# Optimization experiments

Hardware: AMD Instinct MI355X
Metric: run time of the kernel (lower is better)

## Reference

```python
import jax, jax.numpy as jnp
import numpy as np

N = 4096
D = 1024  # hidden_size == att_size


def setup_inputs() -> dict:
    key = jax.random.key(0)
    ks = jax.random.split(key, 10)
    s = 0.02
    return {
        "q": jax.random.normal(ks[0], (N, D), jnp.float32),
        "k": jax.random.normal(ks[1], (N, D), jnp.float32),
        "v": jax.random.normal(ks[2], (N, D), jnp.float32),
        "bias": jax.random.normal(ks[3], (N, N), jnp.float32) * s,
        "Wq": jax.random.normal(ks[4], (D, D), jnp.float32) * s,
        "bq": jnp.zeros((D,), jnp.float32),
        "Wk": jax.random.normal(ks[5], (D, D), jnp.float32) * s,
        "bk": jnp.zeros((D,), jnp.float32),
        "Wv": jax.random.normal(ks[6], (D, D), jnp.float32) * s,
        "bv": jnp.zeros((D,), jnp.float32),
    }


def reference(q, k, v, bias, Wq, bq, Wk, bk, Wv, bv):
    d = q.shape[-1]
    scale = d ** (-0.5)
    # QKV projections (nn.Linear: x @ W.T + b)
    qp = (q @ Wq.T + bq) * scale          # [N, D]
    kp = k @ Wk.T + bk                    # [N, D]
    vp = v @ Wv.T + bv                    # [N, D]
    # full N x N attention (single head, pseudo-batch of 1 in the original)
    scores = qp @ kp.T                    # [N, N]
    att = jax.nn.softmax(scores, axis=-1) + bias  # POST-softmax bias add
    # dropout is identity in eval mode; original casts weights to fp32 here
    out = att.astype(jnp.float32) @ vp    # [N, D]
    return out
```

## Files before the change

### kernel.cpp

```cpp
#include <hip/hip_runtime.h>
#include <hip/hip_bf16.h>
#include <stdint.h>

typedef unsigned short u16;
using bf16x8 = __attribute__((ext_vector_type(8))) __bf16;
using f32x4  = __attribute__((ext_vector_type(4))) float;

__device__ __forceinline__ u16 f2bf(float f) {
    union { float f; unsigned u; } a; a.f = f;
    unsigned u = a.u;
    u += 0x7fffu + ((u >> 16) & 1u);
    return (u16)(u >> 16);
}
__device__ __forceinline__ float bf2f(unsigned bits_hi16) {
    union { unsigned u; float f; } a; a.u = bits_hi16; return a.f;
}

__device__ __forceinline__ void gload_lds16(const void* g, void* l) {
    __builtin_amdgcn_global_load_lds(
        (const __attribute__((address_space(1))) void*)g,
        (__attribute__((address_space(3))) void*)l, 16, 0, 0);
}

__device__ __forceinline__ void xcd_swz(int nx, int ny, int& x, int& y, int& z) {
    const int flat = (int)blockIdx.x + nx * ((int)blockIdx.y + ny * (int)blockIdx.z);
    const int cpx = (nx * ny * (int)gridDim.z) >> 3;
    const int s = (flat & 7) * cpx + (flat >> 3);
    x = s % nx;
    const int t = s / nx;
    y = t % ny;
    z = t / ny;
}

__device__ __forceinline__ void gemm_core(const u16* __restrict__ A,
                                          const u16* __restrict__ B,
                                          int lda, int ldb, int kLen,
                                          int bm, int bn,
                                          u16* sA, u16* sB,
                                          f32x4 acc[4][4])
{
    const int tid  = threadIdx.x;
    const int lane = tid & 63;
    const int wm   = (tid >> 7) & 1;
    const int wn   = (tid >> 6) & 1;

    const u16* Ag0 = A + (long)(bm * 128 + (tid >> 2)) * lda + (tid & 3) * 8;
    const u16* Ag1 = Ag0 + (long)64 * lda;
    const u16* Bg0 = B + (long)(bn * 128 + (tid >> 2)) * ldb + (tid & 3) * 8;
    const u16* Bg1 = Bg0 + (long)64 * ldb;
    u16* la = sA + tid * 8;
    u16* lb = sB + tid * 8;

    const int rfo = (wm * 64 + (lane & 15)) * 32 + (lane >> 4) * 8;
    const int rfoB = (wn * 64 + (lane & 15)) * 32 + (lane >> 4) * 8;

    for (int k0 = 0; k0 < kLen; k0 += 64) {
        gload_lds16(Ag0 + k0, la);
        gload_lds16(Ag1 + k0, la + 2048);
        gload_lds16(Bg0 + k0, lb);
        gload_lds16(Bg1 + k0, lb + 2048);
        gload_lds16(Ag0 + k0 + 32, la + 4096);
        gload_lds16(Ag1 + k0 + 32, la + 6144);
        gload_lds16(Bg0 + k0 + 32, lb + 4096);
        gload_lds16(Bg1 + k0 + 32, lb + 6144);
        __syncthreads();
#pragma unroll
        for (int h = 0; h < 2; h++) {
            const u16* ra = sA + h * 4096 + rfo;
            const u16* rb = sB + h * 4096 + rfoB;
            bf16x8 af[4], bfr[4];
#pragma unroll
            for (int i = 0; i < 4; i++) af[i]  = *(const bf16x8*)(ra + i * 512);
#pragma unroll
            for (int i = 0; i < 4; i++) bfr[i] = *(const bf16x8*)(rb + i * 512);
#pragma unroll
            for (int mi = 0; mi < 4; mi++)
#pragma unroll
                for (int ni = 0; ni < 4; ni++)
                    acc[mi][ni] = __builtin_amdgcn_mfma_f32_16x16x32_bf16(
                        af[mi], bfr[ni], acc[mi][ni], 0, 0, 0);
        }
        __syncthreads();
    }
}

__global__ __launch_bounds__(256)
void cast6(const float* __restrict__ q, const float* __restrict__ k,
           const float* __restrict__ v, const float* __restrict__ wq,
           const float* __restrict__ wk, const float* __restrict__ wv,
           u16* __restrict__ qb, u16* __restrict__ kb, u16* __restrict__ vb,
           u16* __restrict__ wqb, u16* __restrict__ wkb, u16* __restrict__ wvb,
           int nqkv, int nw)
{
    const int z = blockIdx.y;
    const float* s; u16* d; int n;
    switch (z) {
        case 0:  s = q;  d = qb;  n = nqkv; break;
        case 1:  s = k;  d = kb;  n = nqkv; break;
        case 2:  s = v;  d = vb;  n = nqkv; break;
        case 3:  s = wq; d = wqb; n = nw;   break;
        case 4:  s = wk; d = wkb; n = nw;   break;
        default: s = wv; d = wvb; n = nw;   break;
    }
    long i = ((long)blockIdx.x * 256 + threadIdx.x) * 8;
    if (i >= n) return;
    float4 a = *(const float4*)(s + i);
    float4 b = *(const float4*)(s + i + 4);
    ushort4 o0, o1;
    o0.x = f2bf(a.x); o0.y = f2bf(a.y); o0.z = f2bf(a.z); o0.w = f2bf(a.w);
    o1.x = f2bf(b.x); o1.y = f2bf(b.y); o1.z = f2bf(b.z); o1.w = f2bf(b.w);
    *(ushort4*)(d + i)     = o0;
    *(ushort4*)(d + i + 4) = o1;
}

__global__ __launch_bounds__(256, 2)
void proj_gemm(const u16* __restrict__ qb, const u16* __restrict__ kb,
               const u16* __restrict__ vb, const u16* __restrict__ wqb,
               const u16* __restrict__ wkb, const u16* __restrict__ wvb,
               const float* __restrict__ bq, const float* __restrict__ bk,
               const float* __restrict__ bv,
               u16* __restrict__ qp, u16* __restrict__ kp, u16* __restrict__ vpT)
{
    __shared__ __align__(16) u16 sA[8192];
    __shared__ __align__(16) u16 sB[8192];
    int bx, by, bz;
    xcd_swz(8, 32, bx, by, bz);
    const int z = bz;
    const u16* A = (z == 0) ? qb : (z == 1) ? kb : vb;
    const u16* B = (z == 0) ? wqb : (z == 1) ? wkb : wvb;
    const float* bias = (z == 0) ? bq : (z == 1) ? bk : bv;
    u16* OUT = (z == 0) ? qp : (z == 1) ? kp : vpT;
    const float scale = (z == 0) ? 0.03125f : 1.0f;

    f32x4 acc[4][4] = {};
    gemm_core(A, B, 1024, 1024, 1024, by, bx, sA, sB, acc);

    const int lane = threadIdx.x & 63;
    const int wm   = (threadIdx.x >> 7) & 1;
    const int wn   = (threadIdx.x >> 6) & 1;
    const int m0 = by * 128 + wm * 64 + ((lane >> 4) << 2);
    const int n0 = bx * 128 + wn * 64 + (lane & 15);
#pragma unroll
    for (int mi = 0; mi < 4; mi++)
#pragma unroll
        for (int ni = 0; ni < 4; ni++) {
            const int gm = m0 + mi * 16;
            const int gn = n0 + ni * 16;
            const float bb = bias[gn];
#pragma unroll
            for (int r = 0; r < 4; r++) {
                float val = (acc[mi][ni][r] + bb) * scale;
                if (z < 2) OUT[(long)(gm + r) * 1024 + gn] = f2bf(val);
                else       OUT[(long)gn * 4096 + gm + r]   = f2bf(val);
            }
        }
}

__global__ __launch_bounds__(256, 2)
void vproj_gemm(const u16* __restrict__ wvb, const u16* __restrict__ vb,
                const float* __restrict__ bv, u16* __restrict__ vpT)
{
    __shared__ __align__(16) u16 sA[8192];
    __shared__ __align__(16) u16 sB[8192];
    f32x4 acc[4][4] = {};
    gemm_core(wvb, vb, 1024, 1024, 1024, blockIdx.y, blockIdx.x, sA, sB, acc);

    const int lane = threadIdx.x & 63;
    const int wm   = (threadIdx.x >> 7) & 1;
    const int wn   = (threadIdx.x >> 6) & 1;
    const int m0 = blockIdx.y * 128 + wm * 64 + ((lane >> 4) << 2);
    const int n0 = blockIdx.x * 128 + wn * 64 + (lane & 15);
#pragma unroll
    for (int mi = 0; mi < 4; mi++)
#pragma unroll
        for (int ni = 0; ni < 4; ni++) {
            const int gm = m0 + mi * 16;
            const int gn = n0 + ni * 16;
#pragma unroll
            for (int r = 0; r < 4; r++)
                vpT[(long)(gm + r) * 4096 + gn] = f2bf(acc[mi][ni][r] + bv[gm + r]);
        }
}

__global__ __launch_bounds__(256, 2)
void score_gemm(const u16* __restrict__ qp, const u16* __restrict__ kp,
                u16* __restrict__ S)
{
    __shared__ __align__(16) u16 sA[8192];
    __shared__ __align__(16) u16 sB[8192];
    f32x4 acc[4][4] = {};
    gemm_core(qp, kp, 1024, 1024, 1024, blockIdx.y, blockIdx.x, sA, sB, acc);

    const int lane = threadIdx.x & 63;
    const int wm   = (threadIdx.x >> 7) & 1;
    const int wn   = (threadIdx.x >> 6) & 1;
    const int m0 = blockIdx.y * 128 + wm * 64 + ((lane >> 4) << 2);
    const int n0 = blockIdx.x * 128 + wn * 64 + (lane & 15);
#pragma unroll
    for (int mi = 0; mi < 4; mi++)
#pragma unroll
        for (int ni = 0; ni < 4; ni++) {
            const int gm = m0 + mi * 16;
            const int gn = n0 + ni * 16;
#pragma unroll
            for (int r = 0; r < 4; r++)
                S[(long)(gm + r) * 4096 + gn] = f2bf(acc[mi][ni][r]);
        }
}

__global__ __launch_bounds__(256)
void softmax_bias(const u16* __restrict__ S, const float* __restrict__ bias,
                  u16* __restrict__ att)
{
    const long row = blockIdx.x;
    const int tid = threadIdx.x;
    const u16* srow = S + row * 4096 + tid * 16;

    float v[16];
    {
        uint4 a = *(const uint4*)(srow);
        uint4 b = *(const uint4*)(srow + 8);
        unsigned w[8] = {a.x, a.y, a.z, a.w, b.x, b.y, b.z, b.w};
#pragma unroll
        for (int i = 0; i < 8; i++) {
            v[2 * i]     = bf2f(w[i] << 16);
            v[2 * i + 1] = bf2f(w[i] & 0xffff0000u);
        }
    }
    float mx = v[0];
#pragma unroll
    for (int i = 1; i < 16; i++) mx = fmaxf(mx, v[i]);
#pragma unroll
    for (int o = 32; o >= 1; o >>= 1) mx = fmaxf(mx, __shfl_xor(mx, o, 64));
    __shared__ float red[8];
    if ((tid & 63) == 0) red[tid >> 6] = mx;
    __syncthreads();
    mx = fmaxf(fmaxf(red[0], red[1]), fmaxf(red[2], red[3]));
    float sum = 0.f;
#pragma unroll
    for (int i = 0; i < 16; i++) { v[i] = __expf(v[i] - mx); sum += v[i]; }
#pragma unroll
    for (int o = 32; o >= 1; o >>= 1) sum += __shfl_xor(sum, o, 64);
    if ((tid & 63) == 0) red[4 + (tid >> 6)] = sum;
    __syncthreads();
    const float inv = 1.0f / (red[4] + red[5] + red[6] + red[7]);

    const float4* brow = (const float4*)(bias + row * 4096 + tid * 16);
    unsigned o[8];
#pragma unroll
    for (int i = 0; i < 4; i++) {
        float4 b = brow[i];
        unsigned lo = f2bf(v[4 * i + 0] * inv + b.x);
        unsigned hi = f2bf(v[4 * i + 1] * inv + b.y);
        o[2 * i] = lo | (hi << 16);
        lo = f2bf(v[4 * i + 2] * inv + b.z);
        hi = f2bf(v[4 * i + 3] * inv + b.w);
        o[2 * i + 1] = lo | (hi << 16);
    }
    u16* arow = att + row * 4096 + tid * 16;
    *(uint4*)(arow)     = make_uint4(o[0], o[1], o[2], o[3]);
    *(uint4*)(arow + 8) = make_uint4(o[4], o[5], o[6], o[7]);
}

__global__ __launch_bounds__(256, 2)
void out_gemm(const u16* __restrict__ att, const u16* __restrict__ vpT,
              float* __restrict__ P)
{
    __shared__ __align__(16) u16 sA[8192];
    __shared__ __align__(16) u16 sB[8192];
    int bx, by, bz;
    xcd_swz(8, 32, bx, by, bz);
    const u16* A = att + bz * 2048;
    const u16* B = vpT + bz * 2048;
    float* O = P + (long)bz * 4096 * 1024;

    f32x4 acc[4][4] = {};
    gemm_core(A, B, 4096, 4096, 2048, by, bx, sA, sB, acc);

    const int lane = threadIdx.x & 63;
    const int wm   = (threadIdx.x >> 7) & 1;
    const int wn   = (threadIdx.x >> 6) & 1;
    const int m0 = by * 128 + wm * 64 + ((lane >> 4) << 2);
    const int n0 = bx * 128 + wn * 64 + (lane & 15);
#pragma unroll
    for (int mi = 0; mi < 4; mi++)
#pragma unroll
        for (int ni = 0; ni < 4; ni++) {
            const int gm = m0 + mi * 16;
            const int gn = n0 + ni * 16;
#pragma unroll
            for (int r = 0; r < 4; r++)
                O[(long)(gm + r) * 1024 + gn] = acc[mi][ni][r];
        }
}

__global__ __launch_bounds__(256)
void addp(const float* __restrict__ P, float* __restrict__ O)
{
    long i = ((long)blockIdx.x * 256 + threadIdx.x) * 4;
    float4 a = *(const float4*)(P + i);
    float4 b = *(const float4*)(P + 4194304 + i);
    float4 r;
    r.x = a.x + b.x; r.y = a.y + b.y; r.z = a.z + b.z; r.w = a.w + b.w;
    *(float4*)(O + i) = r;
}

extern "C" void kernel_launch(void* const* d_in, const int* in_sizes, int n_in,
                              void* d_out, int out_size, void* d_ws, size_t ws_size,
                              hipStream_t stream)
{
    const float* q    = (const float*)d_in[0];
    const float* k    = (const float*)d_in[1];
    const float* v    = (const float*)d_in[2];
    const float* bias = (const float*)d_in[3];
    const float* Wq   = (const float*)d_in[4];
    const float* bq   = (const float*)d_in[5];
    const float* Wk   = (const float*)d_in[6];
    const float* bk   = (const float*)d_in[7];
    const float* Wv   = (const float*)d_in[8];
    const float* bv   = (const float*)d_in[9];
    float* out = (float*)d_out;

    uint8_t* ws = (uint8_t*)d_ws;
    const size_t MB = 1u << 20;
    u16* qb  = (u16*)(ws);
    u16* kb  = (u16*)(ws + 8 * MB);
    u16* vb  = (u16*)(ws + 16 * MB);
    u16* wqb = (u16*)(ws + 24 * MB);
    u16* wkb = (u16*)(ws + 26 * MB);
    u16* wvb = (u16*)(ws + 28 * MB);
    u16* qp  = (u16*)(ws + 30 * MB);
    u16* kp  = (u16*)(ws + 38 * MB);
    u16* vpT = (u16*)(ws + 46 * MB);
    u16* S   = (u16*)(ws + 54 * MB);
    u16* att = (u16*)(ws);
    float* P = (float*)(ws + 86 * MB);

    cast6<<<dim3(2048, 6), 256, 0, stream>>>(q, k, v, Wq, Wk, Wv,
                                             qb, kb, vb, wqb, wkb, wvb,
                                             4096 * 1024, 1024 * 1024);
    proj_gemm<<<dim3(8, 32, 2), 256, 0, stream>>>(qb, kb, vb, wqb, wkb, wvb,
                                                  bq, bk, bv, qp, kp, vpT);
    vproj_gemm<<<dim3(32, 8), 256, 0, stream>>>(wvb, vb, bv, vpT);
    score_gemm<<<dim3(32, 32), 256, 0, stream>>>(qp, kp, S);
    softmax_bias<<<dim3(4096), 256, 0, stream>>>(S, bias, att);
    out_gemm<<<dim3(8, 32, 2), 256, 0, stream>>>(att, vpT, P);
    addp<<<dim3(4096), 256, 0, stream>>>(P, out);
}
```

Before: 303.6 us.

## Rewrite score GEMM with 256x256 tiles, double-buffered LDS and swizzled fragments

Replaces the 128x128, 256-thread score GEMM with a 256x256, 512-thread kernel. It uses two LDS buffers with loads issued two tiles ahead, XOR-swizzled LDS layout to avoid bank conflicts, an XCD-aware block remap, and MFMA phases interleaved with priority hints. The aim is to raise data reuse per tile and overlap global loads with MFMA compute. In exchange it needs 128KB of LDS and more accumulator registers, and a 256-block grid may underfill the 256 CUs or limit occupancy.

```diff
diff --git a/kernel.cpp b/kernel.cpp
--- a/kernel.cpp
+++ b/kernel.cpp
@@ -51,7 +51,7 @@
     u16* la = sA + tid * 8;
     u16* lb = sB + tid * 8;
 
-    const int rfo = (wm * 64 + (lane & 15)) * 32 + (lane >> 4) * 8;
+    const int rfo  = (wm * 64 + (lane & 15)) * 32 + (lane >> 4) * 8;
     const int rfoB = (wn * 64 + (lane & 15)) * 32 + (lane >> 4) * 8;
 
     for (int k0 = 0; k0 < kLen; k0 += 64) {
@@ -182,26 +182,150 @@
         }
 }
 
-__global__ __launch_bounds__(256, 2)
-void score_gemm(const u16* __restrict__ qp, const u16* __restrict__ kp,
-                u16* __restrict__ S)
-{
-    __shared__ __align__(16) u16 sA[8192];
-    __shared__ __align__(16) u16 sB[8192];
-    f32x4 acc[4][4] = {};
-    gemm_core(qp, kp, 1024, 1024, 1024, blockIdx.y, blockIdx.x, sA, sB, acc);
-
-    const int lane = threadIdx.x & 63;
-    const int wm   = (threadIdx.x >> 7) & 1;
-    const int wn   = (threadIdx.x >> 6) & 1;
-    const int m0 = blockIdx.y * 128 + wm * 64 + ((lane >> 4) << 2);
-    const int n0 = blockIdx.x * 128 + wn * 64 + (lane & 15);
-#pragma unroll
-    for (int mi = 0; mi < 4; mi++)
+__global__ __launch_bounds__(512, 2)
+void score_gemm256(const u16* __restrict__ qp, const u16* __restrict__ kp,
+                   u16* __restrict__ S)
+{
+    __shared__ __align__(16) u16 lds[65536];
+
+    const int flat = (int)blockIdx.x + ((int)blockIdx.y << 4);
+    const int sfl = (flat & 7) * 32 + (flat >> 3);
+    const int bx = sfl & 15;
+    const int by = sfl >> 4;
+
+    const int tid = (int)threadIdx.x;
+    const int l  = tid & 63;
+    const int w  = tid >> 6;
+    const int wm = w >> 2;
+    const int wn = w & 3;
+
+    const int lda = 1024, ldb = 1024;
+    const int T = 16;
+
+    const int srcswz = 8 * ((l & 3) ^ ((l >> 3) & 3));
+    const u16* pA = qp + (long)(by * 256 + w * 32 + (l >> 2)) * lda + srcswz;
+    const u16* pB = kp + (long)(bx * 256 + w * 32 + (l >> 2)) * ldb + srcswz;
+    const int dstbase = w * 1024 + l * 8;
+
+    const int fsw = 8 * ((l >> 4) ^ ((l >> 1) & 3));
+    const int fA = (wm * 128 + (l & 15)) * 32 + fsw;
+    const int fB = (wn * 64  + (l & 15)) * 32 + fsw;
+
+    f32x4 acc[8][4] = {};
+
+    {
+        u16* d0 = lds + dstbase;
+        gload_lds16(pA,                d0);
+        gload_lds16(pA + 16 * lda,     d0 + 512);
+        gload_lds16(pB,                d0 + 16384);
+        gload_lds16(pB + 16 * ldb,     d0 + 16384 + 512);
+        gload_lds16(pA + 32,           d0 + 8192);
+        gload_lds16(pA + 16 * lda + 32, d0 + 8192 + 512);
+        gload_lds16(pB + 32,           d0 + 24576);
+        gload_lds16(pB + 16 * ldb + 32, d0 + 24576 + 512);
+        const u16* a1 = pA + 64;
+        const u16* b1 = pB + 64;
+        u16* d1 = lds + 32768 + dstbase;
+        gload_lds16(a1,                d1);
+        gload_lds16(a1 + 16 * lda,     d1 + 512);
+        gload_lds16(b1,                d1 + 16384);
+        gload_lds16(b1 + 16 * ldb,     d1 + 16384 + 512);
+        gload_lds16(a1 + 32,           d1 + 8192);
+        gload_lds16(a1 + 16 * lda + 32, d1 + 8192 + 512);
+        gload_lds16(b1 + 32,           d1 + 24576);
+        gload_lds16(b1 + 16 * ldb + 32, d1 + 24576 + 512);
+        asm volatile("s_waitcnt vmcnt(8)" ::: "memory");
+        __builtin_amdgcn_s_barrier();
+    }
+
+    for (int t = 0; t < T; ++t) {
+        const int buf = (t & 1) << 15;
+        const u16* Ar = lds + buf;
+        const u16* Br = lds + buf + 16384;
+        const bool st = (t + 2) < T;
+        const u16* sa = pA + (t + 2) * 64;
+        const u16* sb = pB + (t + 2) * 64;
+        u16* d = lds + buf + dstbase;
+
+        bf16x8 af[8], bfr[4];
+
+#pragma unroll
+        for (int mi = 0; mi < 8; mi++)
+            af[mi] = *(const bf16x8*)(Ar + fA + mi * 512);
+#pragma unroll
+        for (int ni = 0; ni < 4; ni++)
+            bfr[ni] = *(const bf16x8*)(Br + fB + ni * 512);
+        __builtin_amdgcn_s_setprio(1);
+#pragma unroll
+        for (int mi = 0; mi < 4; mi++)
+#pragma unroll
+            for (int ni = 0; ni < 4; ni++)
+                acc[mi][ni] = __builtin_amdgcn_mfma_f32_16x16x32_bf16(
+                    af[mi], bfr[ni], acc[mi][ni], 0, 0, 0);
+        __builtin_amdgcn_s_setprio(0);
+        asm volatile("s_waitcnt lgkmcnt(0)" ::: "memory");
+        __builtin_amdgcn_s_barrier();
+
+        if (st) {
+            gload_lds16(sa,            d);
+            gload_lds16(sa + 16 * lda, d + 512);
+            gload_lds16(sb,            d + 16384);
+            gload_lds16(sb + 16 * ldb, d + 16384 + 512);
+        }
+        __builtin_amdgcn_s_setprio(1);
+#pragma unroll
+        for (int mi = 4; mi < 8; mi++)
+#pragma unroll
+            for (int ni = 0; ni < 4; ni++)
+                acc[mi][ni] = __builtin_amdgcn_mfma_f32_16x16x32_bf16(
+                    af[mi], bfr[ni], acc[mi][ni], 0, 0, 0);
+        __builtin_amdgcn_s_setprio(0);
+        __builtin_amdgcn_s_barrier();
+
+#pragma unroll
+        for (int mi = 0; mi < 8; mi++)
+            af[mi] = *(const bf16x8*)(Ar + 8192 + fA + mi * 512);
+#pragma unroll
+        for (int ni = 0; ni < 4; ni++)
+            bfr[ni] = *(const bf16x8*)(Br + 8192 + fB + ni * 512);
+        __builtin_amdgcn_s_setprio(1);
+#pragma unroll
+        for (int mi = 0; mi < 4; mi++)
+#pragma unroll
+            for (int ni = 0; ni < 4; ni++)
+                acc[mi][ni] = __builtin_amdgcn_mfma_f32_16x16x32_bf16(
+                    af[mi], bfr[ni], acc[mi][ni], 0, 0, 0);
+        __builtin_amdgcn_s_setprio(0);
+        asm volatile("s_waitcnt lgkmcnt(0)" ::: "memory");
+        __builtin_amdgcn_s_barrier();
+
+        if (st) {
+            gload_lds16(sa + 32,            d + 8192);
+            gload_lds16(sa + 16 * lda + 32, d + 8192 + 512);
+            gload_lds16(sb + 32,            d + 24576);
+            gload_lds16(sb + 16 * ldb + 32, d + 24576 + 512);
+        }
+        __builtin_amdgcn_s_setprio(1);
+#pragma unroll
+        for (int mi = 4; mi < 8; mi++)
+#pragma unroll
+            for (int ni = 0; ni < 4; ni++)
+                acc[mi][ni] = __builtin_amdgcn_mfma_f32_16x16x32_bf16(
+                    af[mi], bfr[ni], acc[mi][ni], 0, 0, 0);
+        __builtin_amdgcn_s_setprio(0);
+        if (st) asm volatile("s_waitcnt vmcnt(8)" ::: "memory");
+        else    asm volatile("s_waitcnt vmcnt(0)" ::: "memory");
+        __builtin_amdgcn_s_barrier();
+    }
+
+    const int gm0 = by * 256 + wm * 128 + ((l >> 4) << 2);
+    const int gn0 = bx * 256 + wn * 64 + (l & 15);
+#pragma unroll
+    for (int mi = 0; mi < 8; mi++)
 #pragma unroll
         for (int ni = 0; ni < 4; ni++) {
-            const int gm = m0 + mi * 16;
-            const int gn = n0 + ni * 16;
+            const int gm = gm0 + mi * 16;
+            const int gn = gn0 + ni * 16;
 #pragma unroll
             for (int r = 0; r < 4; r++)
                 S[(long)(gm + r) * 4096 + gn] = f2bf(acc[mi][ni][r]);
@@ -342,7 +466,7 @@
     proj_gemm<<<dim3(8, 32, 2), 256, 0, stream>>>(qb, kb, vb, wqb, wkb, wvb,
                                                   bq, bk, bv, qp, kp, vpT);
     vproj_gemm<<<dim3(32, 8), 256, 0, stream>>>(wvb, vb, bv, vpT);
-    score_gemm<<<dim3(32, 32), 256, 0, stream>>>(qp, kp, S);
+    score_gemm256<<<dim3(16, 16), 512, 0, stream>>>(qp, kp, S);
     softmax_bias<<<dim3(4096), 256, 0, stream>>>(S, bias, att);
     out_gemm<<<dim3(8, 32, 2), 256, 0, stream>>>(att, vpT, P);
     addp<<<dim3(4096), 256, 0, stream>>>(P, out);
```

Result: no change. 298.6 us (-1.7%).

## Use 256x256 double-buffered swizzled GEMM core for score and output GEMMs

Applied to the files above, without the earlier changes.

Adds a 256x256-tile GEMM core with 512 threads, double-buffered LDS staging via global_load_lds, XOR-swizzled LDS layout, s_setprio around the MFMA bursts, and manual waitcnt pipelining. The score and output GEMMs both use it, and the output GEMM moves from split-K 2 to split-K 4 with a four-way reduction kernel. The goal is more data reuse per tile and overlap of global loads with MFMA. In exchange it uses 128 KB of LDS per block, puts fewer blocks in flight on the smaller score grid, and writes more partial-sum traffic for split-K 4.

```diff
diff --git a/kernel.cpp b/kernel.cpp
--- a/kernel.cpp
+++ b/kernel.cpp
@@ -51,7 +51,7 @@
     u16* la = sA + tid * 8;
     u16* lb = sB + tid * 8;
 
-    const int rfo = (wm * 64 + (lane & 15)) * 32 + (lane >> 4) * 8;
+    const int rfo  = (wm * 64 + (lane & 15)) * 32 + (lane >> 4) * 8;
     const int rfoB = (wn * 64 + (lane & 15)) * 32 + (lane >> 4) * 8;
 
     for (int k0 = 0; k0 < kLen; k0 += 64) {
@@ -84,6 +84,98 @@
     }
 }
 
+__device__ __forceinline__ void gemm256_core(const u16* __restrict__ A,
+                                             const u16* __restrict__ B,
+                                             int lda, int ldb, int T,
+                                             int rowA0, int rowB0,
+                                             u16* lds,
+                                             f32x4 acc[8][4],
+                                             int wm, int wn)
+{
+    const int tid = (int)threadIdx.x;
+    const int l = tid & 63;
+    const int w = tid >> 6;
+
+    const int srcswz = 8 * ((l & 3) ^ ((l >> 3) & 3));
+    const u16* pA = A + (long)(rowA0 + w * 32 + (l >> 2)) * lda + srcswz;
+    const u16* pB = B + (long)(rowB0 + w * 32 + (l >> 2)) * ldb + srcswz;
+    const int dstbase = w * 1024 + l * 8;
+
+    const int fsw = 8 * ((l >> 4) ^ ((l >> 1) & 3));
+    const int fA = (wm * 128 + (l & 15)) * 32 + fsw;
+    const int fB = (wn * 64  + (l & 15)) * 32 + fsw;
+
+    bf16x8 af0[8], bf0[4], af1[8], bf1[4];
+
+#define STAGE(tile, kh)                                                        \
+    {                                                                          \
+        const long co = (long)(tile) * 64 + (kh) * 32;                         \
+        u16* d = lds + (((tile) & 1) << 15) + ((kh) << 13) + dstbase;          \
+        gload_lds16(pA + co, d);                                               \
+        gload_lds16(pA + co + 16 * (long)lda, d + 512);                        \
+        gload_lds16(pB + co, d + 16384);                                       \
+        gload_lds16(pB + co + 16 * (long)ldb, d + 16384 + 512);                \
+    }
+
+#define RD(af, bfr, tile, ks)                                                  \
+    {                                                                          \
+        const u16* Ar = lds + (((tile) & 1) << 15) + ((ks) << 13);             \
+        const u16* Br = Ar + 16384;                                            \
+        _Pragma("unroll")                                                      \
+        for (int mi = 0; mi < 8; mi++)                                         \
+            af[mi] = *(const bf16x8*)(Ar + fA + mi * 512);                     \
+        _Pragma("unroll")                                                      \
+        for (int ni = 0; ni < 4; ni++)                                         \
+            bfr[ni] = *(const bf16x8*)(Br + fB + ni * 512);                    \
+    }
+
+#define MF(af, bfr, lo)                                                        \
+    {                                                                          \
+        __builtin_amdgcn_s_setprio(1);                                         \
+        _Pragma("unroll")                                                      \
+        for (int mi = (lo); mi < (lo) + 4; mi++)                               \
+            _Pragma("unroll")                                                  \
+            for (int ni = 0; ni < 4; ni++)                                     \
+                acc[mi][ni] = __builtin_amdgcn_mfma_f32_16x16x32_bf16(         \
+                    af[mi], bfr[ni], acc[mi][ni], 0, 0, 0);                    \
+        __builtin_amdgcn_s_setprio(0);                                         \
+    }
+
+    STAGE(0, 0); STAGE(0, 1); STAGE(1, 0); STAGE(1, 1);
+    asm volatile("s_waitcnt vmcnt(8)" ::: "memory");
+    __builtin_amdgcn_s_barrier();
+    RD(af0, bf0, 0, 0);
+    asm volatile("s_waitcnt lgkmcnt(0)" ::: "memory");
+    __builtin_amdgcn_s_barrier();
+
+    for (int t = 0; t < T; ++t) {
+        const int t2  = (t + 2 < T) ? t + 2 : T - 1;
+        const int t1c = (t + 1 < T) ? t + 1 : T - 1;
+
+        RD(af1, bf1, t, 1);
+        MF(af0, bf0, 0);
+
+        STAGE(t2, 0);
+        MF(af0, bf0, 4);
+        asm volatile("s_waitcnt lgkmcnt(0)" ::: "memory");
+        __builtin_amdgcn_s_barrier();
+
+        asm volatile("s_waitcnt vmcnt(4)" ::: "memory");
+        RD(af0, bf0, t1c, 0);
+        MF(af1, bf1, 0);
+
+        STAGE(t2, 1);
+        MF(af1, bf1, 4);
+        asm volatile("s_waitcnt lgkmcnt(0)" ::: "memory");
+        __builtin_amdgcn_s_barrier();
+    }
+    asm volatile("s_waitcnt vmcnt(0)" ::: "memory");
+
+#undef STAGE
+#undef RD
+#undef MF
+}
+
 __global__ __launch_bounds__(256)
 void cast6(const float* __restrict__ q, const float* __restrict__ k,
            const float* __restrict__ v, const float* __restrict__ wq,
@@ -182,26 +274,33 @@
         }
 }
 
-__global__ __launch_bounds__(256, 2)
-void score_gemm(const u16* __restrict__ qp, const u16* __restrict__ kp,
-                u16* __restrict__ S)
-{
-    __shared__ __align__(16) u16 sA[8192];
-    __shared__ __align__(16) u16 sB[8192];
-    f32x4 acc[4][4] = {};
-    gemm_core(qp, kp, 1024, 1024, 1024, blockIdx.y, blockIdx.x, sA, sB, acc);
-
-    const int lane = threadIdx.x & 63;
-    const int wm   = (threadIdx.x >> 7) & 1;
-    const int wn   = (threadIdx.x >> 6) & 1;
-    const int m0 = blockIdx.y * 128 + wm * 64 + ((lane >> 4) << 2);
-    const int n0 = blockIdx.x * 128 + wn * 64 + (lane & 15);
-#pragma unroll
-    for (int mi = 0; mi < 4; mi++)
+__global__ __launch_bounds__(512, 2)
+void score_gemm256(const u16* __restrict__ qp, const u16* __restrict__ kp,
+                   u16* __restrict__ S)
+{
+    __shared__ __align__(16) u16 lds[65536];
+
+    const int flat = (int)blockIdx.x + ((int)blockIdx.y << 4);
+    const int sfl = (flat & 7) * 32 + (flat >> 3);
+    const int bx = sfl & 15;
+    const int by = sfl >> 4;
+
+    const int l  = (int)threadIdx.x & 63;
+    const int w  = (int)threadIdx.x >> 6;
+    const int wm = w >> 2;
+    const int wn = w & 3;
+
+    f32x4 acc[8][4] = {};
+    gemm256_core(qp, kp, 1024, 1024, 16, by * 256, bx * 256, lds, acc, wm, wn);
+
+    const int gm0 = by * 256 + wm * 128 + ((l >> 4) << 2);
+    const int gn0 = bx * 256 + wn * 64 + (l & 15);
+#pragma unroll
+    for (int mi = 0; mi < 8; mi++)
 #pragma unroll
         for (int ni = 0; ni < 4; ni++) {
-            const int gm = m0 + mi * 16;
-            const int gn = n0 + ni * 16;
+            const int gm = gm0 + mi * 16;
+            const int gn = gn0 + ni * 16;
 #pragma unroll
             for (int r = 0; r < 4; r++)
                 S[(long)(gm + r) * 4096 + gn] = f2bf(acc[mi][ni][r]);
@@ -262,32 +361,34 @@
     *(uint4*)(arow + 8) = make_uint4(o[4], o[5], o[6], o[7]);
 }
 
-__global__ __launch_bounds__(256, 2)
-void out_gemm(const u16* __restrict__ att, const u16* __restrict__ vpT,
-              float* __restrict__ P)
-{
-    __shared__ __align__(16) u16 sA[8192];
-    __shared__ __align__(16) u16 sB[8192];
+__global__ __launch_bounds__(512, 2)
+void out_gemm256(const u16* __restrict__ att, const u16* __restrict__ vpT,
+                 float* __restrict__ P)
+{
+    __shared__ __align__(16) u16 lds[65536];
+
     int bx, by, bz;
-    xcd_swz(8, 32, bx, by, bz);
-    const u16* A = att + bz * 2048;
-    const u16* B = vpT + bz * 2048;
+    xcd_swz(4, 16, bx, by, bz);
+    const u16* A = att + bz * 1024;
+    const u16* B = vpT + bz * 1024;
     float* O = P + (long)bz * 4096 * 1024;
 
-    f32x4 acc[4][4] = {};
-    gemm_core(A, B, 4096, 4096, 2048, by, bx, sA, sB, acc);
-
-    const int lane = threadIdx.x & 63;
-    const int wm   = (threadIdx.x >> 7) & 1;
-    const int wn   = (threadIdx.x >> 6) & 1;
-    const int m0 = by * 128 + wm * 64 + ((lane >> 4) << 2);
-    const int n0 = bx * 128 + wn * 64 + (lane & 15);
-#pragma unroll
-    for (int mi = 0; mi < 4; mi++)
+    const int l  = (int)threadIdx.x & 63;
+    const int w  = (int)threadIdx.x >> 6;
+    const int wm = w >> 2;
+    const int wn = w & 3;
+
+    f32x4 acc[8][4] = {};
+    gemm256_core(A, B, 4096, 4096, 16, by * 256, bx * 256, lds, acc, wm, wn);
+
+    const int gm0 = by * 256 + wm * 128 + ((l >> 4) << 2);
+    const int gn0 = bx * 256 + wn * 64 + (l & 15);
+#pragma unroll
+    for (int mi = 0; mi < 8; mi++)
 #pragma unroll
         for (int ni = 0; ni < 4; ni++) {
-            const int gm = m0 + mi * 16;
-            const int gn = n0 + ni * 16;
+            const int gm = gm0 + mi * 16;
+            const int gn = gn0 + ni * 16;
 #pragma unroll
             for (int r = 0; r < 4; r++)
                 O[(long)(gm + r) * 1024 + gn] = acc[mi][ni][r];
@@ -295,13 +396,19 @@
 }
 
 __global__ __launch_bounds__(256)
-void addp(const float* __restrict__ P, float* __restrict__ O)
+void addp4(const float* __restrict__ P, float* __restrict__ O)
 {
     long i = ((long)blockIdx.x * 256 + threadIdx.x) * 4;
+    const long st = 4194304;
     float4 a = *(const float4*)(P + i);
-    float4 b = *(const float4*)(P + 4194304 + i);
+    float4 b = *(const float4*)(P + st + i);
+    float4 c = *(const float4*)(P + 2 * st + i);
+    float4 d = *(const float4*)(P + 3 * st + i);
     float4 r;
-    r.x = a.x + b.x; r.y = a.y + b.y; r.z = a.z + b.z; r.w = a.w + b.w;
+    r.x = (a.x + b.x) + (c.x + d.x);
+    r.y = (a.y + b.y) + (c.y + d.y);
+    r.z = (a.z + b.z) + (c.z + d.z);
+    r.w = (a.w + b.w) + (c.w + d.w);
     *(float4*)(O + i) = r;
 }
 
@@ -334,7 +441,7 @@
     u16* vpT = (u16*)(ws + 46 * MB);
     u16* S   = (u16*)(ws + 54 * MB);
     u16* att = (u16*)(ws);
-    float* P = (float*)(ws + 86 * MB);
+    float* P = (float*)(ws + 54 * MB);
 
     cast6<<<dim3(2048, 6), 256, 0, stream>>>(q, k, v, Wq, Wk, Wv,
                                              qb, kb, vb, wqb, wkb, wvb,
@@ -342,8 +449,8 @@
     proj_gemm<<<dim3(8, 32, 2), 256, 0, stream>>>(qb, kb, vb, wqb, wkb, wvb,
                                                   bq, bk, bv, qp, kp, vpT);
     vproj_gemm<<<dim3(32, 8), 256, 0, stream>>>(wvb, vb, bv, vpT);
-    score_gemm<<<dim3(32, 32), 256, 0, stream>>>(qp, kp, S);
+    score_gemm256<<<dim3(16, 16), 512, 0, stream>>>(qp, kp, S);
     softmax_bias<<<dim3(4096), 256, 0, stream>>>(S, bias, att);
-    out_gemm<<<dim3(8, 32, 2), 256, 0, stream>>>(att, vpT, P);
-    addp<<<dim3(4096), 256, 0, stream>>>(P, out);
-}
+    out_gemm256<<<dim3(4, 16, 4), 512, 0, stream>>>(att, vpT, P);
+    addp4<<<dim3(4096), 256, 0, stream>>>(P, out);
+}
```

Result: no change. 302.7 us (-0.3%).
